# Optimization experiments

Measured on AMD Instinct MI355X. Metric: run time of the kernel, lower is better.

## Reference

```python
import jax, jax.numpy as jnp
import numpy as np

B, T, K, H = 2, 4096, 512, 8


def setup_inputs() -> dict:
    key = jax.random.key(0)
    ks = jax.random.split(key, 6)
    scale = 1.0 / np.sqrt(K)
    return {
        "x": jax.random.normal(ks[0], (B, T, K), dtype=jnp.float32),
        "padding_mask": jnp.ones((B, T), dtype=jnp.int32),
        "Wq": jax.random.normal(ks[1], (K, K), dtype=jnp.float32) * scale,
        "Wk": jax.random.normal(ks[2], (K, K), dtype=jnp.float32) * scale,
        "Wv": jax.random.normal(ks[3], (K, K), dtype=jnp.float32) * scale,
        "Wu": jax.random.normal(ks[4], (K, K), dtype=jnp.float32) * scale,
        "bu": jnp.zeros((K,), dtype=jnp.float32),
    }


def reference(x, padding_mask, Wq, Wk, Wv, Wu, bu):
    b, t, e = x.shape
    h = H
    s = e // h
    # torch Linear: y = x @ W.T
    q = (x @ Wq.T).reshape(b, t, h, s).transpose(0, 2, 1, 3)  # (b,h,t,s)
    k = (x @ Wk.T).reshape(b, t, h, s).transpose(0, 2, 1, 3)
    v = (x @ Wv.T).reshape(b, t, h, s).transpose(0, 2, 1, 3)
    inv4 = e ** (-0.25)
    q = q * inv4
    k = k * inv4
    dot = jnp.einsum("bhqs,bhks->bhqk", q, k)  # (b,h,t,t)
    neg_inf = jnp.float32(-jnp.inf)
    # causal mask (self.mask == True)
    causal = jnp.triu(jnp.ones((t, t), dtype=bool), k=1)
    dot = jnp.where(causal[None, None], neg_inf, dot)
    # padding mask applied along the QUERY dimension, as in the original
    dot = jnp.where(padding_mask[:, None, :, None] == 0, neg_inf, dot)
    attn = jax.nn.softmax(dot, axis=-1)
    out = jnp.einsum("bhqk,bhks->bhqs", attn, v)  # (b,h,t,s)
    out = out.transpose(0, 2, 1, 3).reshape(b, t, e)
    return out @ Wu.T + bu
```

## Files before the change

kernel.cpp:

```cpp
#include <hip/hip_runtime.h>
#include <hip/hip_bf16.h>

#define BB 2
#define TT 4096
#define KK 512
#define HH 8
#define SS 64
#define MM 8192

typedef __attribute__((ext_vector_type(8))) short bf16x8;
typedef __attribute__((ext_vector_type(4))) float f32x4;
typedef unsigned int u32;
typedef __attribute__((ext_vector_type(2))) u32 u32x2;
typedef __attribute__((ext_vector_type(4))) u32 u32x4;

#define SCL_QK 0.25250488f

static __device__ __forceinline__ short f2b(float f) {
    union { float f; unsigned u; } v;
    v.f = f;
    unsigned r = v.u + 0x7fffu + ((v.u >> 16) & 1u);
    return (short)(r >> 16);
}

static __device__ __forceinline__ u32 cvt2(float lo, float hi) {
    u32 r;
    asm("v_cvt_pk_bf16_f32 %0, %1, %2" : "=v"(r) : "v"(lo), "v"(hi));
    return r;
}

#define GLOAD16(g, l) __builtin_amdgcn_global_load_lds( \
    (const __attribute__((address_space(1))) void*)(g), \
    (__attribute__((address_space(3))) void*)(l), 16, 0, 0)

__global__ __launch_bounds__(256) void cvt_bf16(
    const float* __restrict__ x,
    const float* __restrict__ Wq, const float* __restrict__ Wk,
    const float* __restrict__ Wv, const float* __restrict__ Wu,
    short* __restrict__ xb, short* __restrict__ wb)
{
    const int NX = MM * KK;
    const int NW = KK * KK;
    int idx = blockIdx.x * blockDim.x + threadIdx.x;
    int total = (NX + 4 * NW) >> 3;
    for (int g = idx; g < total; g += gridDim.x * blockDim.x) {
        int e = g << 3;
        const float* src; short* dst;
        if (e < NX) { src = x + e; dst = xb + e; }
        else {
            int gg = e - NX;
            int wsel = gg >> 18;
            int off = gg & (NW - 1);
            src = (wsel == 0 ? Wq : wsel == 1 ? Wk : wsel == 2 ? Wv : Wu) + off;
            dst = wb + gg;
        }
        float4 a = *(const float4*)src;
        float4 b = *(const float4*)(src + 4);
        u32x4 wv = { cvt2(a.x, a.y), cvt2(a.z, a.w), cvt2(b.x, b.y), cvt2(b.z, b.w) };
        *(u32x4*)dst = wv;
    }
}

__global__ __launch_bounds__(256) void proj_qkv(
    const short* __restrict__ xb, const short* __restrict__ wb,
    short* __restrict__ q, short* __restrict__ k, short* __restrict__ v)
{
    __shared__ short aS[128 * 64];
    __shared__ short bS[128 * 64];
    int nt = blockIdx.x, mt = blockIdx.y, z = blockIdx.z;
    const short* W = wb + (size_t)z * KK * KK;
    short* dst = (z == 0) ? q : ((z == 1) ? k : v);
    int tid = threadIdx.x, wave = tid >> 6, lane = tid & 63;
    int lr = lane & 15, lg = lane >> 4;
    int wr = wave >> 1, wc = wave & 1;
    int l8 = lane >> 3, c8 = lane & 7;

    const short* Ag = xb + (size_t)(mt * 128) * KK;
    const short* Bg = W + (size_t)(nt * 128) * KK;

    f32x4 acc[4][4];
#pragma unroll
    for (int m = 0; m < 4; ++m)
#pragma unroll
        for (int n = 0; n < 4; ++n) acc[m][n] = (f32x4){0.f, 0.f, 0.f, 0.f};

    for (int k0 = 0; k0 < KK; k0 += 64) {
        __syncthreads();
#pragma unroll
        for (int i = 0; i < 4; ++i) {
            int row = wave * 32 + i * 8 + l8;
            GLOAD16(Ag + (size_t)row * KK + k0 + c8 * 8, &aS[(wave * 32 + i * 8) * 64]);
            GLOAD16(Bg + (size_t)row * KK + k0 + c8 * 8, &bS[(wave * 32 + i * 8) * 64]);
        }
        __syncthreads();
#pragma unroll
        for (int kc = 0; kc < 2; ++kc) {
            bf16x8 af[4], bw[4];
#pragma unroll
            for (int m = 0; m < 4; ++m)
                af[m] = *(const bf16x8*)&aS[(wr * 64 + m * 16 + lr) * 64 + kc * 32 + lg * 8];
#pragma unroll
            for (int n = 0; n < 4; ++n)
                bw[n] = *(const bf16x8*)&bS[(wc * 64 + n * 16 + lr) * 64 + kc * 32 + lg * 8];
#pragma unroll
            for (int m = 0; m < 4; ++m)
#pragma unroll
                for (int n = 0; n < 4; ++n)
                    acc[m][n] = __builtin_amdgcn_mfma_f32_16x16x32_bf16(af[m], bw[n], acc[m][n], 0, 0, 0);
        }
    }

#pragma unroll
    for (int n = 0; n < 4; ++n) {
        int nn = nt * 128 + wc * 64 + n * 16 + lr;
        int h = nn >> 6, s = nn & 63;
#pragma unroll
        for (int m = 0; m < 4; ++m) {
            int m0 = mt * 128 + wr * 64 + m * 16 + lg * 4;
            int b = m0 >> 12, t0 = m0 & (TT - 1);
            if (z == 2) {
                u32x2 pk = { cvt2(acc[m][n][0], acc[m][n][1]), cvt2(acc[m][n][2], acc[m][n][3]) };
                *(u32x2*)&dst[(((size_t)(b * HH + h)) * SS + s) * TT + t0] = pk;
            } else {
#pragma unroll
                for (int r = 0; r < 4; ++r)
                    dst[(((size_t)(b * HH + h)) * TT + (t0 + r)) * SS + s] = f2b(acc[m][n][r] * SCL_QK);
            }
        }
    }
}

__global__ __launch_bounds__(256) void proj_out(
    const short* __restrict__ a, const short* __restrict__ Wub,
    const float* __restrict__ bu, float* __restrict__ out)
{
    __shared__ short aS[64 * 64];
    __shared__ short bS[128 * 64];
    int nt = blockIdx.x, mt = blockIdx.y;
    int tid = threadIdx.x, wave = tid >> 6, lane = tid & 63;
    int lr = lane & 15, lg = lane >> 4;
    int wr = wave >> 1, wc = wave & 1;
    int l8 = lane >> 3, c8 = lane & 7;

    const short* Ag = a + (size_t)(mt * 64) * KK;
    const short* Bg = Wub + (size_t)(nt * 128) * KK;

    f32x4 acc[2][4];
#pragma unroll
    for (int m = 0; m < 2; ++m)
#pragma unroll
        for (int n = 0; n < 4; ++n) acc[m][n] = (f32x4){0.f, 0.f, 0.f, 0.f};

    for (int k0 = 0; k0 < KK; k0 += 64) {
        __syncthreads();
#pragma unroll
        for (int i = 0; i < 2; ++i) {
            int row = wave * 16 + i * 8 + l8;
            GLOAD16(Ag + (size_t)row * KK + k0 + c8 * 8, &aS[(wave * 16 + i * 8) * 64]);
        }
#pragma unroll
        for (int i = 0; i < 4; ++i) {
            int row = wave * 32 + i * 8 + l8;
            GLOAD16(Bg + (size_t)row * KK + k0 + c8 * 8, &bS[(wave * 32 + i * 8) * 64]);
        }
        __syncthreads();
#pragma unroll
        for (int kc = 0; kc < 2; ++kc) {
            bf16x8 af[2], bw[4];
#pragma unroll
            for (int m = 0; m < 2; ++m)
                af[m] = *(const bf16x8*)&aS[(wr * 32 + m * 16 + lr) * 64 + kc * 32 + lg * 8];
#pragma unroll
            for (int n = 0; n < 4; ++n)
                bw[n] = *(const bf16x8*)&bS[(wc * 64 + n * 16 + lr) * 64 + kc * 32 + lg * 8];
#pragma unroll
            for (int m = 0; m < 2; ++m)
#pragma unroll
                for (int n = 0; n < 4; ++n)
                    acc[m][n] = __builtin_amdgcn_mfma_f32_16x16x32_bf16(af[m], bw[n], acc[m][n], 0, 0, 0);
        }
    }

#pragma unroll
    for (int n = 0; n < 4; ++n) {
        int nn = nt * 128 + wc * 64 + n * 16 + lr;
        float bias = bu[nn];
#pragma unroll
        for (int m = 0; m < 2; ++m) {
            int mm = mt * 64 + wr * 32 + m * 16 + lg * 4;
#pragma unroll
            for (int r = 0; r < 4; ++r)
                out[(size_t)(mm + r) * KK + nn] = acc[m][n][r] + bias;
        }
    }
}

__global__ __launch_bounds__(256) void flash_attn(
    const short* __restrict__ Q, const short* __restrict__ Kv,
    const short* __restrict__ Vt, short* __restrict__ Oout)
{
    __shared__ short k_lds[64][72];
    __shared__ short v_lds[64][72];
    __shared__ short p_lds[4][16][72];

    int u = blockIdx.x;
    int i = u & 15, bh = (u >> 4) & 15, j = u >> 8;
    int sl = j * 16 + i;
    int qt = (sl < 16) ? (63 - sl) : (sl < 32 ? (sl - 16) : (sl < 48 ? (79 - sl) : (sl - 32)));

    int tid = threadIdx.x, wave = tid >> 6, lane = tid & 63;
    int lr = lane & 15, lg = lane >> 4;
    int b = bh >> 3, h = bh & 7;

    const short* Qb = Q + (size_t)bh * TT * SS;
    const short* Kb = Kv + (size_t)bh * TT * SS;
    const short* Vb = Vt + (size_t)bh * SS * TT;

    int urow = tid >> 3, useg = tid & 7;

    int qrow0 = qt * 64 + wave * 16;

    bf16x8 a_q[2];
#pragma unroll
    for (int kc = 0; kc < 2; ++kc)
        a_q[kc] = *(const bf16x8*)&Qb[(size_t)(qrow0 + lr) * SS + kc * 32 + lg * 8];

    f32x4 o[4];
#pragma unroll
    for (int n = 0; n < 4; ++n) o[n] = (f32x4){0.f, 0.f, 0.f, 0.f};
    float m_run = -INFINITY, l_run = 0.f;

    int nkv = qt + 1;
    bf16x8 kr0, kr1, vr0, vr1;
    kr0 = *(const bf16x8*)&Kb[(size_t)urow * SS + useg * 8];
    kr1 = *(const bf16x8*)&Kb[(size_t)(urow + 32) * SS + useg * 8];
    vr0 = *(const bf16x8*)&Vb[(size_t)urow * TT + useg * 8];
    vr1 = *(const bf16x8*)&Vb[(size_t)(urow + 32) * TT + useg * 8];

    for (int kt = 0; kt < nkv; ++kt) {
        __syncthreads();
        *(bf16x8*)&k_lds[urow][useg * 8]      = kr0;
        *(bf16x8*)&k_lds[urow + 32][useg * 8] = kr1;
        *(bf16x8*)&v_lds[urow][useg * 8]      = vr0;
        *(bf16x8*)&v_lds[urow + 32][useg * 8] = vr1;
        if (kt + 1 < nkv) {
            int kn = kt + 1;
            kr0 = *(const bf16x8*)&Kb[(size_t)(kn * 64 + urow) * SS + useg * 8];
            kr1 = *(const bf16x8*)&Kb[(size_t)(kn * 64 + urow + 32) * SS + useg * 8];
            vr0 = *(const bf16x8*)&Vb[(size_t)urow * TT + kn * 64 + useg * 8];
            vr1 = *(const bf16x8*)&Vb[(size_t)(urow + 32) * TT + kn * 64 + useg * 8];
        }
        __syncthreads();

        f32x4 sc[4];
#pragma unroll
        for (int ct = 0; ct < 4; ++ct) sc[ct] = (f32x4){0.f, 0.f, 0.f, 0.f};
        __builtin_amdgcn_s_setprio(1);
#pragma unroll
        for (int kc = 0; kc < 2; ++kc) {
#pragma unroll
            for (int ct = 0; ct < 4; ++ct) {
                bf16x8 kf = *(const bf16x8*)&k_lds[ct * 16 + lr][kc * 32 + lg * 8];
                sc[ct] = __builtin_amdgcn_mfma_f32_16x16x32_bf16(kf, a_q[kc], sc[ct], 0, 0, 0);
            }
        }
        __builtin_amdgcn_s_setprio(0);
        if (kt == qt) {
#pragma unroll
            for (int ct = 0; ct < 4; ++ct) {
                int kv0 = kt * 64 + ct * 16 + lg * 4;
                int qq = qrow0 + lr;
#pragma unroll
                for (int r = 0; r < 4; ++r)
                    if (kv0 + r > qq) sc[ct][r] = -INFINITY;
            }
        }
        float mx = -INFINITY;
#pragma unroll
        for (int ct = 0; ct < 4; ++ct)
#pragma unroll
            for (int r = 0; r < 4; ++r) mx = fmaxf(mx, sc[ct][r]);
        mx = fmaxf(mx, __shfl_xor(mx, 16));
        mx = fmaxf(mx, __shfl_xor(mx, 32));
        if (!__all(mx <= m_run + 8.0f)) {
            float mnew = fmaxf(m_run, mx);
            float corr = __builtin_amdgcn_exp2f(m_run - mnew);
            l_run *= corr;
#pragma unroll
            for (int st = 0; st < 4; ++st)
#pragma unroll
                for (int r = 0; r < 4; ++r) o[st][r] *= corr;
            m_run = mnew;
        }
        float s0 = 0.f;
#pragma unroll
        for (int ct = 0; ct < 4; ++ct)
#pragma unroll
            for (int r = 0; r < 4; ++r) {
                float pf = __builtin_amdgcn_exp2f(sc[ct][r] - m_run);
                sc[ct][r] = pf;
                s0 += pf;
            }
        s0 += __shfl_xor(s0, 16);
        s0 += __shfl_xor(s0, 32);
        l_run += s0;

#pragma unroll
        for (int ct = 0; ct < 4; ++ct) {
            u32x2 pk = { cvt2(sc[ct][0], sc[ct][1]), cvt2(sc[ct][2], sc[ct][3]) };
            *(u32x2*)&p_lds[wave][lr][ct * 16 + lg * 4] = pk;
        }
        asm volatile("s_waitcnt lgkmcnt(0)" ::: "memory");
        __builtin_amdgcn_s_setprio(1);
#pragma unroll
        for (int kc = 0; kc < 2; ++kc) {
            bf16x8 pb = *(const bf16x8*)&p_lds[wave][lr][kc * 32 + lg * 8];
#pragma unroll
            for (int st = 0; st < 4; ++st) {
                bf16x8 vf = *(const bf16x8*)&v_lds[st * 16 + lr][kc * 32 + lg * 8];
                o[st] = __builtin_amdgcn_mfma_f32_16x16x32_bf16(vf, pb, o[st], 0, 0, 0);
            }
        }
        __builtin_amdgcn_s_setprio(0);
    }

    float inv = 1.f / l_run;
    int t = qrow0 + lr;
#pragma unroll
    for (int st = 0; st < 4; ++st) {
        u32x2 ov = { cvt2(o[st][0] * inv, o[st][1] * inv), cvt2(o[st][2] * inv, o[st][3] * inv) };
        *(u32x2*)&Oout[(size_t)(b * TT + t) * KK + h * 64 + st * 16 + lg * 4] = ov;
    }
}

extern "C" void kernel_launch(void* const* d_in, const int* in_sizes, int n_in,
                              void* d_out, int out_size, void* d_ws, size_t ws_size,
                              hipStream_t stream) {
    const float* x  = (const float*)d_in[0];
    const float* Wq = (const float*)d_in[2];
    const float* Wk = (const float*)d_in[3];
    const float* Wv = (const float*)d_in[4];
    const float* Wu = (const float*)d_in[5];
    const float* bu = (const float*)d_in[6];
    float* out = (float*)d_out;

    short* q_ws  = (short*)d_ws;
    short* k_ws  = q_ws + (size_t)MM * KK;
    short* v_ws  = k_ws + (size_t)MM * KK;
    short* a_ws  = v_ws + (size_t)MM * KK;
    short* wb_ws = a_ws + (size_t)MM * KK;

    cvt_bf16<<<2560, 256, 0, stream>>>(x, Wq, Wk, Wv, Wu, a_ws, wb_ws);

    dim3 gQKV(KK / 128, MM / 128, 3);
    proj_qkv<<<gQKV, 256, 0, stream>>>(a_ws, wb_ws, q_ws, k_ws, v_ws);

    flash_attn<<<1024, 256, 0, stream>>>(q_ws, k_ws, v_ws, a_ws);

    dim3 gO(KK / 128, MM / 64);
    proj_out<<<gO, 256, 0, stream>>>(a_ws, wb_ws + 3 * (size_t)KK * KK, bu, out);
}
```

Before: 200.8 us.

## Keep attention probabilities in registers via permuted K layout, fold QK scale into weights

The flash attention kernel stores K rows in LDS under a bit permutation, so the score MFMA output lanes already match the B-operand layout for the PV MFMA. This removes the P round trip through LDS and its wait. The QK scale is folded into the bf16 weight conversion, and the Q/K/out projections swap MFMA operands so epilogues write packed vector stores instead of scalar ones. The block-to-(bh, q-tile) mapping is also changed to group heads per XCD, which depends on the hardware assigning blocks to XCDs round-robin.

```diff
diff --git a/kernel.cpp b/kernel.cpp
--- a/kernel.cpp
+++ b/kernel.cpp
@@ -16,13 +16,6 @@
 
 #define SCL_QK 0.25250488f
 
-static __device__ __forceinline__ short f2b(float f) {
-    union { float f; unsigned u; } v;
-    v.f = f;
-    unsigned r = v.u + 0x7fffu + ((v.u >> 16) & 1u);
-    return (short)(r >> 16);
-}
-
 static __device__ __forceinline__ u32 cvt2(float lo, float hi) {
     u32 r;
     asm("v_cvt_pk_bf16_f32 %0, %1, %2" : "=v"(r) : "v"(lo), "v"(hi));
@@ -32,6 +25,10 @@
 #define GLOAD16(g, l) __builtin_amdgcn_global_load_lds( \
     (const __attribute__((address_space(1))) void*)(g), \
     (__attribute__((address_space(3))) void*)(l), 16, 0, 0)
+
+static __device__ __forceinline__ int rho(int v) {
+    return (v & 0x23) | ((v & 0x04) << 2) | ((v & 0x18) >> 1);
+}
 
 __global__ __launch_bounds__(256) void cvt_bf16(
     const float* __restrict__ x,
@@ -45,7 +42,7 @@
     int total = (NX + 4 * NW) >> 3;
     for (int g = idx; g < total; g += gridDim.x * blockDim.x) {
         int e = g << 3;
-        const float* src; short* dst;
+        const float* src; short* dst; float scl = 1.0f;
         if (e < NX) { src = x + e; dst = xb + e; }
         else {
             int gg = e - NX;
@@ -53,9 +50,12 @@
             int off = gg & (NW - 1);
             src = (wsel == 0 ? Wq : wsel == 1 ? Wk : wsel == 2 ? Wv : Wu) + off;
             dst = wb + gg;
+            if (wsel <= 1) scl = SCL_QK;
         }
         float4 a = *(const float4*)src;
         float4 b = *(const float4*)(src + 4);
+        a.x *= scl; a.y *= scl; a.z *= scl; a.w *= scl;
+        b.x *= scl; b.y *= scl; b.z *= scl; b.w *= scl;
         u32x4 wv = { cvt2(a.x, a.y), cvt2(a.z, a.w), cvt2(b.x, b.y), cvt2(b.z, b.w) };
         *(u32x4*)dst = wv;
     }
@@ -70,6 +70,7 @@
     int nt = blockIdx.x, mt = blockIdx.y, z = blockIdx.z;
     const short* W = wb + (size_t)z * KK * KK;
     short* dst = (z == 0) ? q : ((z == 1) ? k : v);
+    bool tr = (z != 2);
     int tid = threadIdx.x, wave = tid >> 6, lane = tid & 63;
     int lr = lane & 15, lg = lane >> 4;
     int wr = wave >> 1, wc = wave & 1;
@@ -102,29 +103,46 @@
 #pragma unroll
             for (int n = 0; n < 4; ++n)
                 bw[n] = *(const bf16x8*)&bS[(wc * 64 + n * 16 + lr) * 64 + kc * 32 + lg * 8];
-#pragma unroll
-            for (int m = 0; m < 4; ++m)
-#pragma unroll
-                for (int n = 0; n < 4; ++n)
-                    acc[m][n] = __builtin_amdgcn_mfma_f32_16x16x32_bf16(af[m], bw[n], acc[m][n], 0, 0, 0);
-        }
-    }
-
-#pragma unroll
-    for (int n = 0; n < 4; ++n) {
-        int nn = nt * 128 + wc * 64 + n * 16 + lr;
-        int h = nn >> 6, s = nn & 63;
-#pragma unroll
-        for (int m = 0; m < 4; ++m) {
-            int m0 = mt * 128 + wr * 64 + m * 16 + lg * 4;
-            int b = m0 >> 12, t0 = m0 & (TT - 1);
-            if (z == 2) {
+            if (tr) {
+#pragma unroll
+                for (int m = 0; m < 4; ++m)
+#pragma unroll
+                    for (int n = 0; n < 4; ++n)
+                        acc[m][n] = __builtin_amdgcn_mfma_f32_16x16x32_bf16(bw[n], af[m], acc[m][n], 0, 0, 0);
+            } else {
+#pragma unroll
+                for (int m = 0; m < 4; ++m)
+#pragma unroll
+                    for (int n = 0; n < 4; ++n)
+                        acc[m][n] = __builtin_amdgcn_mfma_f32_16x16x32_bf16(af[m], bw[n], acc[m][n], 0, 0, 0);
+            }
+        }
+    }
+
+    if (tr) {
+        int h = nt * 2 + wc;
+#pragma unroll
+        for (int n = 0; n < 4; ++n) {
+            int s0 = n * 16 + lg * 4;
+#pragma unroll
+            for (int m = 0; m < 4; ++m) {
+                int tg = mt * 128 + wr * 64 + m * 16 + lr;
+                int b = tg >> 12, t = tg & (TT - 1);
+                u32x2 pk = { cvt2(acc[m][n][0], acc[m][n][1]), cvt2(acc[m][n][2], acc[m][n][3]) };
+                *(u32x2*)&dst[((size_t)(b * HH + h) * TT + t) * SS + s0] = pk;
+            }
+        }
+    } else {
+#pragma unroll
+        for (int n = 0; n < 4; ++n) {
+            int nn = nt * 128 + wc * 64 + n * 16 + lr;
+            int h = nn >> 6, s = nn & 63;
+#pragma unroll
+            for (int m = 0; m < 4; ++m) {
+                int m0 = mt * 128 + wr * 64 + m * 16 + lg * 4;
+                int b = m0 >> 12, t0 = m0 & (TT - 1);
                 u32x2 pk = { cvt2(acc[m][n][0], acc[m][n][1]), cvt2(acc[m][n][2], acc[m][n][3]) };
                 *(u32x2*)&dst[(((size_t)(b * HH + h)) * SS + s) * TT + t0] = pk;
-            } else {
-#pragma unroll
-                for (int r = 0; r < 4; ++r)
-                    dst[(((size_t)(b * HH + h)) * TT + (t0 + r)) * SS + s] = f2b(acc[m][n][r] * SCL_QK);
             }
         }
     }
@@ -177,20 +195,20 @@
             for (int m = 0; m < 2; ++m)
 #pragma unroll
                 for (int n = 0; n < 4; ++n)
-                    acc[m][n] = __builtin_amdgcn_mfma_f32_16x16x32_bf16(af[m], bw[n], acc[m][n], 0, 0, 0);
+                    acc[m][n] = __builtin_amdgcn_mfma_f32_16x16x32_bf16(bw[n], af[m], acc[m][n], 0, 0, 0);
         }
     }
 
 #pragma unroll
     for (int n = 0; n < 4; ++n) {
-        int nn = nt * 128 + wc * 64 + n * 16 + lr;
-        float bias = bu[nn];
+        int f0 = nt * 128 + wc * 64 + n * 16 + lg * 4;
+        float4 bias4 = *(const float4*)&bu[f0];
 #pragma unroll
         for (int m = 0; m < 2; ++m) {
-            int mm = mt * 64 + wr * 32 + m * 16 + lg * 4;
-#pragma unroll
-            for (int r = 0; r < 4; ++r)
-                out[(size_t)(mm + r) * KK + nn] = acc[m][n][r] + bias;
+            int t = mt * 64 + wr * 32 + m * 16 + lr;
+            float4 ov = { acc[m][n][0] + bias4.x, acc[m][n][1] + bias4.y,
+                          acc[m][n][2] + bias4.z, acc[m][n][3] + bias4.w };
+            *(float4*)&out[(size_t)t * KK + f0] = ov;
         }
     }
 }
@@ -201,12 +219,12 @@
 {
     __shared__ short k_lds[64][72];
     __shared__ short v_lds[64][72];
-    __shared__ short p_lds[4][16][72];
 
     int u = blockIdx.x;
-    int i = u & 15, bh = (u >> 4) & 15, j = u >> 8;
-    int sl = j * 16 + i;
-    int qt = (sl < 16) ? (63 - sl) : (sl < 32 ? (sl - 16) : (sl < 48 ? (79 - sl) : (sl - 32)));
+    int xcd = u & 7, sblk = u >> 3;
+    int bh = 2 * xcd + (sblk & 1);
+    int i4 = sblk >> 1;
+    int qt = (i4 < 16) ? (63 - i4) : (i4 < 32 ? (i4 - 16) : (i4 < 48 ? (79 - i4) : (i4 - 32)));
 
     int tid = threadIdx.x, wave = tid >> 6, lane = tid & 63;
     int lr = lane & 15, lg = lane >> 4;
@@ -217,6 +235,7 @@
     const short* Vb = Vt + (size_t)bh * SS * TT;
 
     int urow = tid >> 3, useg = tid & 7;
+    int kdr0 = rho(urow), kdr1 = rho(urow + 32);
 
     int qrow0 = qt * 64 + wave * 16;
 
@@ -239,8 +258,8 @@
 
     for (int kt = 0; kt < nkv; ++kt) {
         __syncthreads();
-        *(bf16x8*)&k_lds[urow][useg * 8]      = kr0;
-        *(bf16x8*)&k_lds[urow + 32][useg * 8] = kr1;
+        *(bf16x8*)&k_lds[kdr0][useg * 8]      = kr0;
+        *(bf16x8*)&k_lds[kdr1][useg * 8]      = kr1;
         *(bf16x8*)&v_lds[urow][useg * 8]      = vr0;
         *(bf16x8*)&v_lds[urow + 32][useg * 8] = vr1;
         if (kt + 1 < nkv) {
@@ -266,10 +285,10 @@
         }
         __builtin_amdgcn_s_setprio(0);
         if (kt == qt) {
+            int qq = qrow0 + lr;
 #pragma unroll
             for (int ct = 0; ct < 4; ++ct) {
-                int kv0 = kt * 64 + ct * 16 + lg * 4;
-                int qq = qrow0 + lr;
+                int kv0 = kt * 64 + (ct >> 1) * 32 + lg * 8 + (ct & 1) * 4;
 #pragma unroll
                 for (int r = 0; r < 4; ++r)
                     if (kv0 + r > qq) sc[ct][r] = -INFINITY;
@@ -305,16 +324,14 @@
         s0 += __shfl_xor(s0, 32);
         l_run += s0;
 
-#pragma unroll
-        for (int ct = 0; ct < 4; ++ct) {
-            u32x2 pk = { cvt2(sc[ct][0], sc[ct][1]), cvt2(sc[ct][2], sc[ct][3]) };
-            *(u32x2*)&p_lds[wave][lr][ct * 16 + lg * 4] = pk;
-        }
-        asm volatile("s_waitcnt lgkmcnt(0)" ::: "memory");
         __builtin_amdgcn_s_setprio(1);
 #pragma unroll
         for (int kc = 0; kc < 2; ++kc) {
-            bf16x8 pb = *(const bf16x8*)&p_lds[wave][lr][kc * 32 + lg * 8];
+            u32x4 pw = { cvt2(sc[2 * kc][0], sc[2 * kc][1]),
+                         cvt2(sc[2 * kc][2], sc[2 * kc][3]),
+                         cvt2(sc[2 * kc + 1][0], sc[2 * kc + 1][1]),
+                         cvt2(sc[2 * kc + 1][2], sc[2 * kc + 1][3]) };
+            bf16x8 pb = __builtin_bit_cast(bf16x8, pw);
 #pragma unroll
             for (int st = 0; st < 4; ++st) {
                 bf16x8 vf = *(const bf16x8*)&v_lds[st * 16 + lr][kc * 32 + lg * 8];
```

Result: faster. 192.1 us (-4.4%).
